# Kernel optimization log

Hardware: AMD Instinct MI355X
Metric: run time of the kernel (lower is better)

Reference implementation:

```python
import jax, jax.numpy as jnp
import numpy as np

C = 256
NUM_HEADS = 8
HEAD_DIM = C // NUM_HEADS
SCALE = HEAD_DIM ** -0.5


def setup_inputs() -> dict:
    key = jax.random.key(0)
    ks = jax.random.split(key, 10)
    B, H, W = 2, 64, 64
    s = 0.02
    return {
        "spatial_feat": jax.random.normal(ks[0], (B, C, H, W), jnp.float32),
        "freq_feat": jax.random.normal(ks[1], (B, C, H, W), jnp.float32),
        "wq": jax.random.normal(ks[2], (C, C), jnp.float32) * s,
        "bq": jax.random.normal(ks[3], (C,), jnp.float32) * s,
        "wk": jax.random.normal(ks[4], (C, C), jnp.float32) * s,
        "bk": jax.random.normal(ks[5], (C,), jnp.float32) * s,
        "wv": jax.random.normal(ks[6], (C, C), jnp.float32) * s,
        "bv": jax.random.normal(ks[7], (C,), jnp.float32) * s,
        "wo": jax.random.normal(ks[8], (C, C), jnp.float32) * s,
        "bo": jax.random.normal(ks[9], (C,), jnp.float32) * s,
    }


def _proj(x, w, b):
    # 1x1 conv == channel-mixing matmul: (O,C) x (B,C,H,W) -> (B,O,H,W)
    return jnp.einsum('oc,bchw->bohw', w, x) + b[None, :, None, None]


def _heads(x, B, HW):
    return x.reshape(B, NUM_HEADS, HEAD_DIM, HW)


def _cross_attend(q_src, kv_src, wq, bq, wk, bk, wv, bv, wo, bo):
    B, Cc, H, W = q_src.shape
    HW = H * W
    q = _heads(_proj(q_src, wq, bq), B, HW)   # (B, h, d, N)
    k = _heads(_proj(kv_src, wk, bk), B, HW)
    v = _heads(_proj(kv_src, wv, bv), B, HW)
    # attn[b,h,m,n] = q[...,m] . k[...,n]
    attn = jnp.einsum('bhdm,bhdn->bhmn', q, k) * SCALE
    attn = jax.nn.softmax(attn, axis=-1)
    # out[...,m] = sum_n v[...,n] * attn[m,n]
    out = jnp.einsum('bhdn,bhmn->bhdm', v, attn)
    out = out.reshape(B, Cc, H, W)
    return _proj(out, wo, bo)


def reference(spatial_feat, freq_feat, wq, bq, wk, bk, wv, bv, wo, bo):
    spatial_attended = spatial_feat + _cross_attend(
        spatial_feat, freq_feat, wq, bq, wk, bk, wv, bv, wo, bo)
    freq_attended = freq_feat + _cross_attend(
        freq_feat, spatial_feat, wq, bq, wk, bk, wv, bv, wo, bo)
    return spatial_attended + freq_attended
```

## Files before the change

kernel.cpp:

```cpp
#include <hip/hip_runtime.h>
#include <hip/hip_bf16.h>

#define B_ 2
#define C_ 256
#define NH_ 8
#define D_ 32
#define N_ 4096
#define SCALE_ 0.17677669529663689f
#define QSC_ 0.25505277f

typedef __hip_bfloat16 bf16;
typedef __attribute__((ext_vector_type(8))) short sx8;
typedef __attribute__((ext_vector_type(4))) short sx4;
typedef __attribute__((ext_vector_type(4))) float fx4;
typedef __attribute__((ext_vector_type(4))) int ix4;

__device__ __forceinline__ float b2f(bf16 x) { return __bfloat162float(x); }
__device__ __forceinline__ bf16 f2b(float x) { return __float2bfloat16(x); }
__device__ __forceinline__ short fbs(float x) { bf16 h = __float2bfloat16(x); return *(short*)&h; }
__device__ __forceinline__ float sbf(short s) { bf16 h = *(bf16*)&s; return __bfloat162float(h); }

#if __has_builtin(__builtin_amdgcn_exp2f)
__device__ __forceinline__ float fexp2(float x) { return __builtin_amdgcn_exp2f(x); }
#else
__device__ __forceinline__ float fexp2(float x) { return exp2f(x); }
#endif

__device__ __forceinline__ unsigned pkbf_tr(float x, float y) {
#if __has_builtin(__builtin_amdgcn_perm)
  return __builtin_amdgcn_perm(__builtin_bit_cast(unsigned, y),
                               __builtin_bit_cast(unsigned, x), 0x07060302u);
#else
  unsigned a = __builtin_bit_cast(unsigned, x) >> 16;
  unsigned b = __builtin_bit_cast(unsigned, y) & 0xFFFF0000u;
  return a | b;
#endif
}
__device__ __forceinline__ void pl32swap(unsigned &a, unsigned &b) {
  asm volatile("v_permlane32_swap_b32 %0, %1" : "+v"(a), "+v"(b));
}
__device__ __forceinline__ void pl16swap(unsigned &a, unsigned &b) {
  asm volatile("v_permlane16_swap_b32 %0, %1" : "+v"(a), "+v"(b));
}

__global__ __launch_bounds__(256)
void convert_kernel(const float* __restrict__ spatial,
                    const float* __restrict__ freq,
                    const float* __restrict__ wq, const float* __restrict__ wk,
                    const float* __restrict__ wv, const float* __restrict__ wo,
                    bf16* __restrict__ xb, bf16* __restrict__ wb,
                    bf16* __restrict__ wob) {
  const int tid = threadIdx.x;
  if (blockIdx.z == 4) {
    int base = (blockIdx.y * 64 + blockIdx.x) * 256 + tid;
    #pragma unroll
    for (int i = 0; i < 4; ++i) {
      int idx = base + i * 65536;
      if (idx < 196608) {
        const float* src = (idx < 65536) ? wq : (idx < 131072) ? wk : wv;
        wb[idx] = f2b(src[idx & 65535]);
      } else {
        wob[idx - 196608] = f2b(wo[idx - 196608]);
      }
    }
    return;
  }

  const int p0 = blockIdx.x * 64;
  const int c0 = blockIdx.y * 64;
  const int z  = blockIdx.z;
  const int s = z >> 1, b = z & 1;
  const float* x = (s == 0) ? spatial : freq;

  __shared__ float ls[64][65];

  const int pp = tid & 63, cb = tid >> 6;
  #pragma unroll
  for (int i = 0; i < 16; ++i) {
    int c = cb + 4 * i;
    ls[c][pp] = x[(size_t)(b * C_ + c0 + c) * N_ + p0 + pp];
  }
  __syncthreads();

  #pragma unroll
  for (int i = 0; i < 2; ++i) {
    int j = tid + 256 * i;
    int p = j >> 3, ck = (j & 7) * 8;
    short tmp[8];
    #pragma unroll
    for (int u = 0; u < 8; ++u) tmp[u] = fbs(ls[ck + u][p]);
    *(sx8*)(xb + ((size_t)z * N_ + p0 + p) * C_ + c0 + ck) = *(sx8*)tmp;
  }
}

__global__ __launch_bounds__(256)
void qkv_gemm_kernel(const bf16* __restrict__ wb, const bf16* __restrict__ xb,
                     const float* __restrict__ bq, const float* __restrict__ bk,
                     const float* __restrict__ bv,
                     bf16* __restrict__ qhf, bf16* __restrict__ khf,
                     bf16* __restrict__ vhf) {
  const int tid = threadIdx.x;
  const int p0 = blockIdx.x * 128;
  const int o0 = blockIdx.y * 128;
  const int z  = blockIdx.z;

  const int lane = tid & 63, w = tid >> 6;
  const int ml = lane & 15, Q4 = (lane >> 4) * 4, Q8 = (lane >> 4) * 8;
  const int ow = (w >> 1) * 64, pw = (w & 1) * 64;

  __shared__ __align__(16) short smem[2 * 128 * 72];
  short* asb = smem;
  short* bsb = smem + 128 * 72;
  __shared__ float bias_s[128];

  if (tid < 128) {
    int o = o0 + tid;
    bias_s[tid] = (o < 256) ? bq[o] : (o < 512) ? bk[o - 256] : bv[o - 512];
  }

  const fx4 z4 = {0.f, 0.f, 0.f, 0.f};
  fx4 acc[4][4];
  #pragma unroll
  for (int ot = 0; ot < 4; ++ot)
    #pragma unroll
    for (int pt = 0; pt < 4; ++pt) acc[ot][pt] = z4;

  const int sr = tid >> 1, scu = (tid & 1) * 32;
  for (int k0 = 0; k0 < 256; k0 += 64) {
    __syncthreads();
    #pragma unroll
    for (int u = 0; u < 4; ++u) {
      *(sx8*)&asb[sr * 72 + scu + u * 8] =
          *(const sx8*)&wb[(o0 + sr) * 256 + k0 + scu + u * 8];
      *(sx8*)&bsb[sr * 72 + scu + u * 8] =
          *(const sx8*)(xb + ((size_t)z * N_ + p0 + sr) * C_ + k0 + scu + u * 8);
    }
    __syncthreads();
    #pragma unroll
    for (int kk = 0; kk < 2; ++kk) {
      sx8 af[4], bfr[4];
      #pragma unroll
      for (int t = 0; t < 4; ++t)
        af[t] = *(sx8*)&asb[(ow + t * 16 + ml) * 72 + kk * 32 + Q8];
      #pragma unroll
      for (int t = 0; t < 4; ++t)
        bfr[t] = *(sx8*)&bsb[(pw + t * 16 + ml) * 72 + kk * 32 + Q8];
      #pragma unroll
      for (int ot = 0; ot < 4; ++ot)
        #pragma unroll
        for (int pt = 0; pt < 4; ++pt)
          acc[ot][pt] = __builtin_amdgcn_mfma_f32_16x16x32_bf16(
              af[ot], bfr[pt], acc[ot][pt], 0, 0, 0);
    }
  }

  if (o0 < 512) {
    bf16* dst = (o0 < 256) ? qhf : khf;
    const int ob = (o0 < 256) ? o0 : o0 - 256;
    const float scl = (o0 < 256) ? QSC_ : 1.f;
    #pragma unroll
    for (int ot = 0; ot < 4; ++ot) {
      const int og = ob + ow + ot * 16 + Q4;
      #pragma unroll
      for (int pt = 0; pt < 4; ++pt) {
        int p = p0 + pw + pt * 16 + ml;
        short tmp[4];
        #pragma unroll
        for (int r = 0; r < 4; ++r)
          tmp[r] = fbs((acc[ot][pt][r] + bias_s[ow + ot * 16 + Q4 + r]) * scl);
        *(sx4*)(dst + (((size_t)z * NH_ + (og >> 5)) * N_ + p) * D_ + (og & 31)) =
            *(sx4*)tmp;
      }
    }
  } else {
    __syncthreads();
    #pragma unroll
    for (int ot = 0; ot < 4; ++ot)
      #pragma unroll
      for (int pt = 0; pt < 4; ++pt) {
        int pl = pw + pt * 16 + ml;
        #pragma unroll
        for (int r = 0; r < 4; ++r) {
          int lo = ow + ot * 16 + Q4 + r;
          smem[lo * 136 + pl] = fbs(acc[ot][pt][r] + bias_s[lo]);
        }
      }
    __syncthreads();
    const int rho0 = o0 - 512;
    #pragma unroll
    for (int i = 0; i < 8; ++i) {
      int j = tid + 256 * i;
      int lo = j >> 4, pg = j & 15;
      int rho = rho0 + lo;
      int h = rho >> 5, d = rho & 31;
      int p = p0 + pg * 8;
      size_t basev = ((size_t)z * NH_ + h) * D_ * N_;
      sx8 v = *(sx8*)&smem[lo * 136 + pg * 8];
      *(sx8*)(vhf + basev + (size_t)(p >> 5) * 1024 + (d >> 4) * 512 +
              (d & 15) * 32 + (p & 31)) = v;
    }
  }
}

__device__ __forceinline__ void attn_tile(const sx8 kf[4], const sx8 vf[2][2],
                                          const sx8 qf[4], sx8 onesf,
                                          fx4 acc[4][2], fx4 lacc[4]) {
  const fx4 z4 = {0.f, 0.f, 0.f, 0.f};
  #pragma unroll
  for (int s4 = 0; s4 < 4; ++s4) {
    fx4 st[4];
    __builtin_amdgcn_s_setprio(1);
    #pragma unroll
    for (int t = 0; t < 4; ++t)
      st[t] = __builtin_amdgcn_mfma_f32_16x16x32_bf16(kf[t], qf[s4], z4, 0, 0, 0);
    __builtin_amdgcn_s_setprio(0);

    unsigned T[4][2];
    #pragma unroll
    for (int t = 0; t < 4; ++t) {
      float e0 = fexp2(st[t][0]), e1 = fexp2(st[t][1]);
      float e2 = fexp2(st[t][2]), e3 = fexp2(st[t][3]);
      T[t][0] = pkbf_tr(e0, e1);
      T[t][1] = pkbf_tr(e2, e3);
    }
    pl32swap(T[0][0], T[1][0]); pl16swap(T[0][0], T[1][0]);
    pl32swap(T[0][1], T[1][1]); pl16swap(T[0][1], T[1][1]);
    pl32swap(T[2][0], T[3][0]); pl16swap(T[2][0], T[3][0]);
    pl32swap(T[2][1], T[3][1]); pl16swap(T[2][1], T[3][1]);
    ix4 p0 = {(int)T[0][0], (int)T[0][1], (int)T[1][0], (int)T[1][1]};
    ix4 p1 = {(int)T[2][0], (int)T[2][1], (int)T[3][0], (int)T[3][1]};
    sx8 pf0 = *(sx8*)&p0;
    sx8 pf1 = *(sx8*)&p1;

    __builtin_amdgcn_s_setprio(1);
    lacc[s4] = __builtin_amdgcn_mfma_f32_16x16x32_bf16(onesf, pf0, lacc[s4], 0, 0, 0);
    lacc[s4] = __builtin_amdgcn_mfma_f32_16x16x32_bf16(onesf, pf1, lacc[s4], 0, 0, 0);
    #pragma unroll
    for (int dt = 0; dt < 2; ++dt) {
      fx4 a = acc[s4][dt];
      a = __builtin_amdgcn_mfma_f32_16x16x32_bf16(vf[dt][0], pf0, a, 0, 0, 0);
      a = __builtin_amdgcn_mfma_f32_16x16x32_bf16(vf[dt][1], pf1, a, 0, 0, 0);
      acc[s4][dt] = a;
    }
    __builtin_amdgcn_s_setprio(0);
  }
}

__global__ __launch_bounds__(256, 2)
void attn_kernel(const bf16* __restrict__ qhf, const bf16* __restrict__ khf,
                 const bf16* __restrict__ vhf, bf16* __restrict__ attoT) {
  const int tid  = threadIdx.x;
  const int m0   = blockIdx.x * 256;
  const int h    = blockIdx.y;
  const int z    = blockIdx.z;
  const int s = z >> 1, b = z & 1;
  const int zo = ((1 - s) << 1) | b;

  const bf16* qz = qhf + ((size_t)z  * NH_ + h) * N_ * D_;
  const bf16* kz = khf + ((size_t)zo * NH_ + h) * N_ * D_;
  const bf16* vz = vhf + ((size_t)zo * NH_ + h) * D_ * N_;

  const int lane = tid & 63;
  const int w    = tid >> 6;
  const int ml   = lane & 15;
  const int q4   = lane >> 4;
  const int Q4   = q4 * 4;
  const int Q8   = q4 * 8;

  sx8 qf[4];
  #pragma unroll
  for (int s4 = 0; s4 < 4; ++s4)
    qf[s4] = *(const sx8*)(qz + (size_t)(m0 + w * 64 + s4 * 16 + ml) * D_ + Q8);

  sx8 onesf;
  #pragma unroll
  for (int u = 0; u < 8; ++u) onesf[u] = (short)0x3F80;

  const fx4 z4 = {0.f, 0.f, 0.f, 0.f};
  fx4 acc[4][2];
  #pragma unroll
  for (int s4 = 0; s4 < 4; ++s4) { acc[s4][0] = z4; acc[s4][1] = z4; }
  fx4 lacc[4] = {z4, z4, z4, z4};

  const bf16* kbase = kz + (size_t)ml * D_ + Q8;
  const bf16* vbase = vz + (size_t)ml * 32 + Q8;

#define LDK(n0, kf)                                                          \
  {                                                                          \
    _Pragma("unroll") for (int t = 0; t < 4; ++t)                            \
        kf[t] = *(const sx8*)(kbase + (size_t)((n0) + t * 16) * D_);         \
  }
#define LDV(n0, vf)                                                          \
  {                                                                          \
    _Pragma("unroll") for (int dt = 0; dt < 2; ++dt)                         \
        _Pragma("unroll") for (int c = 0; c < 2; ++c)                        \
            vf[dt][c] = *(const sx8*)(vbase +                                \
                (size_t)(((n0) >> 5) + c) * 1024 + dt * 512);                \
  }

  sx8 kfA[4], kfB[4], vfA[2][2], vfB[2][2];
  LDK(0, kfA);
  LDV(0, vfA);

  #pragma unroll 1
  for (int n0 = 0; n0 < N_; n0 += 128) {
    const int nn = n0 + 64;
    LDK(nn, kfB);
    LDV(nn, vfB);
    attn_tile(kfA, vfA, qf, onesf, acc, lacc);

    const int nn2 = (nn + 64 < N_) ? nn + 64 : 0;
    LDK(nn2, kfA);
    LDV(nn2, vfA);
    attn_tile(kfB, vfB, qf, onesf, acc, lacc);
  }
#undef LDK
#undef LDV

  #pragma unroll
  for (int s4 = 0; s4 < 4; ++s4) {
    float inv = 1.f / lacc[s4][0];
    int col = m0 + w * 64 + s4 * 16 + ml;
    #pragma unroll
    for (int dt = 0; dt < 2; ++dt) {
      short tmp[4];
      #pragma unroll
      for (int r = 0; r < 4; ++r) tmp[r] = fbs(acc[s4][dt][r] * inv);
      *(sx4*)(attoT + ((size_t)z * N_ + col) * C_ + h * D_ + dt * 16 + Q4) =
          *(sx4*)tmp;
    }
  }
}

__global__ __launch_bounds__(256)
void out_proj_kernel(const bf16* __restrict__ wob, const bf16* __restrict__ attoT,
                     const float* __restrict__ spatial,
                     const float* __restrict__ freq,
                     const float* __restrict__ bo, float* __restrict__ out) {
  const int tid = threadIdx.x;
  const int p0 = blockIdx.x * 64;
  const int o0 = blockIdx.y * 64;
  const int b  = blockIdx.z;

  const int lane = tid & 63, w = tid >> 6;
  const int ml = lane & 15, Q4 = (lane >> 4) * 4, Q8 = (lane >> 4) * 8;
  const int ow = (w >> 1) * 32, pw = (w & 1) * 32;

  __shared__ __align__(16) short asb[64 * 72];
  __shared__ __align__(16) short bsb[64 * 72];
  __shared__ float bo_s[64];

  if (tid < 64) bo_s[tid] = 2.f * bo[o0 + tid];

  const bf16* at0 = attoT + (size_t)(0 + b) * N_ * C_;
  const bf16* at1 = attoT + (size_t)(2 + b) * N_ * C_;

  const fx4 z4 = {0.f, 0.f, 0.f, 0.f};
  fx4 acc[2][2];
  #pragma unroll
  for (int ot = 0; ot < 2; ++ot)
    #pragma unroll
    for (int pt = 0; pt < 2; ++pt) acc[ot][pt] = z4;

  for (int k0 = 0; k0 < 256; k0 += 64) {
    __syncthreads();
    #pragma unroll
    for (int i = 0; i < 2; ++i) {
      int j = tid + 256 * i;
      int r = j >> 3, cu = (j & 7) * 8;
      *(sx8*)&asb[r * 72 + cu] = *(const sx8*)&wob[(o0 + r) * 256 + k0 + cu];
      sx8 va = *(const sx8*)(at0 + (size_t)(p0 + r) * C_ + k0 + cu);
      sx8 vb2 = *(const sx8*)(at1 + (size_t)(p0 + r) * C_ + k0 + cu);
      short tmp[8];
      #pragma unroll
      for (int u = 0; u < 8; ++u) tmp[u] = fbs(sbf(va[u]) + sbf(vb2[u]));
      *(sx8*)&bsb[r * 72 + cu] = *(sx8*)tmp;
    }
    __syncthreads();
    #pragma unroll
    for (int kk = 0; kk < 2; ++kk) {
      sx8 af[2], bfr[2];
      #pragma unroll
      for (int t = 0; t < 2; ++t)
        af[t] = *(sx8*)&asb[(ow + t * 16 + ml) * 72 + kk * 32 + Q8];
      #pragma unroll
      for (int t = 0; t < 2; ++t)
        bfr[t] = *(sx8*)&bsb[(pw + t * 16 + ml) * 72 + kk * 32 + Q8];
      #pragma unroll
      for (int ot = 0; ot < 2; ++ot)
        #pragma unroll
        for (int pt = 0; pt < 2; ++pt)
          acc[ot][pt] = __builtin_amdgcn_mfma_f32_16x16x32_bf16(
              af[ot], bfr[pt], acc[ot][pt], 0, 0, 0);
    }
  }

  #pragma unroll
  for (int ot = 0; ot < 2; ++ot)
    #pragma unroll
    for (int pt = 0; pt < 2; ++pt) {
      int p = p0 + pw + pt * 16 + ml;
      #pragma unroll
      for (int r = 0; r < 4; ++r) {
        int ol = ow + ot * 16 + Q4 + r;
        size_t off = ((size_t)b * C_ + o0 + ol) * N_ + p;
        out[off] = acc[ot][pt][r] + bo_s[ol] + spatial[off] + freq[off];
      }
    }
}

extern "C" void kernel_launch(void* const* d_in, const int* in_sizes, int n_in,
                              void* d_out, int out_size, void* d_ws, size_t ws_size,
                              hipStream_t stream) {
  const float* spatial = (const float*)d_in[0];
  const float* freq    = (const float*)d_in[1];
  const float* wq = (const float*)d_in[2];
  const float* bq = (const float*)d_in[3];
  const float* wk = (const float*)d_in[4];
  const float* bk = (const float*)d_in[5];
  const float* wv = (const float*)d_in[6];
  const float* bv = (const float*)d_in[7];
  const float* wo = (const float*)d_in[8];
  const float* bo = (const float*)d_in[9];
  float* out = (float*)d_out;

  const size_t SZ = (size_t)2 * B_ * N_ * C_;
  bf16* xb    = (bf16*)d_ws;
  bf16* qhf   = xb + SZ;
  bf16* khf   = qhf + SZ;
  bf16* vhf   = khf + SZ;
  bf16* attoT = vhf + SZ;
  bf16* wb    = attoT + SZ;
  bf16* wob   = wb + 768 * 256;

  convert_kernel<<<dim3(N_ / 64, C_ / 64, 5), 256, 0, stream>>>(
      spatial, freq, wq, wk, wv, wo, xb, wb, wob);
  qkv_gemm_kernel<<<dim3(N_ / 128, 768 / 128, 2 * B_), 256, 0, stream>>>(
      wb, xb, bq, bk, bv, qhf, khf, vhf);
  attn_kernel<<<dim3(N_ / 256, NH_, 2 * B_), 256, 0, stream>>>(
      qhf, khf, vhf, attoT);
  out_proj_kernel<<<dim3(N_ / 64, C_ / 64, B_), 256, 0, stream>>>(
      wob, attoT, spatial, freq, bo, out);
}
```

Baseline: 189.2 us.

## Pre-tile QKV GEMM operands into MFMA fragment layout and load directly from global

The convert kernel now writes the bf16 weights and activations in a 16x32 tiled layout that matches the MFMA fragment order. The QKV GEMM then drops its LDS staging and barriers and loads fragments straight from global memory, double-buffering them in registers across the K chunks. It also adds an occupancy hint of 3 blocks per CU. This removes LDS traffic and synchronisation, but every wave now fetches its own operands from global/L2 with less reuse, and the register pressure rises.

Measured after the change: 193.7 us. 2.4% more time.

```diff
diff --git a/kernel.cpp b/kernel.cpp
--- a/kernel.cpp
+++ b/kernel.cpp
@@ -42,6 +42,7 @@
 __device__ __forceinline__ void pl16swap(unsigned &a, unsigned &b) {
   asm volatile("v_permlane16_swap_b32 %0, %1" : "+v"(a), "+v"(b));
 }
+
 
 __global__ __launch_bounds__(256)
 void convert_kernel(const float* __restrict__ spatial,
@@ -58,7 +59,9 @@
       int idx = base + i * 65536;
       if (idx < 196608) {
         const float* src = (idx < 65536) ? wq : (idx < 131072) ? wk : wv;
-        wb[idx] = f2b(src[idx & 65535]);
+        int o = idx >> 8, c = idx & 255;
+        wb[((o >> 4) * 8 + (c >> 5)) * 512 + (o & 15) * 32 + (c & 31)] =
+            f2b(src[idx & 65535]);
       } else {
         wob[idx - 196608] = f2b(wo[idx - 196608]);
       }
@@ -86,14 +89,17 @@
   for (int i = 0; i < 2; ++i) {
     int j = tid + 256 * i;
     int p = j >> 3, ck = (j & 7) * 8;
+    int pg = p0 + p, cg = c0 + ck;
     short tmp[8];
     #pragma unroll
     for (int u = 0; u < 8; ++u) tmp[u] = fbs(ls[ck + u][p]);
-    *(sx8*)(xb + ((size_t)z * N_ + p0 + p) * C_ + c0 + ck) = *(sx8*)tmp;
-  }
-}
-
-__global__ __launch_bounds__(256)
+    *(sx8*)(xb + (size_t)z * N_ * C_ +
+            (size_t)(((pg >> 4) * 8 + (cg >> 5)) * 512) +
+            (pg & 15) * 32 + (cg & 31)) = *(sx8*)tmp;
+  }
+}
+
+__global__ __launch_bounds__(256, 3)
 void qkv_gemm_kernel(const bf16* __restrict__ wb, const bf16* __restrict__ xb,
                      const float* __restrict__ bq, const float* __restrict__ bk,
                      const float* __restrict__ bv,
@@ -108,9 +114,7 @@
   const int ml = lane & 15, Q4 = (lane >> 4) * 4, Q8 = (lane >> 4) * 8;
   const int ow = (w >> 1) * 64, pw = (w & 1) * 64;
 
-  __shared__ __align__(16) short smem[2 * 128 * 72];
-  short* asb = smem;
-  short* bsb = smem + 128 * 72;
+  __shared__ __align__(16) short esm[128 * 136];
   __shared__ float bias_s[128];
 
   if (tid < 128) {
@@ -125,34 +129,41 @@
     #pragma unroll
     for (int pt = 0; pt < 4; ++pt) acc[ot][pt] = z4;
 
-  const int sr = tid >> 1, scu = (tid & 1) * 32;
-  for (int k0 = 0; k0 < 256; k0 += 64) {
-    __syncthreads();
-    #pragma unroll
-    for (int u = 0; u < 4; ++u) {
-      *(sx8*)&asb[sr * 72 + scu + u * 8] =
-          *(const sx8*)&wb[(o0 + sr) * 256 + k0 + scu + u * 8];
-      *(sx8*)&bsb[sr * 72 + scu + u * 8] =
-          *(const sx8*)(xb + ((size_t)z * N_ + p0 + sr) * C_ + k0 + scu + u * 8);
-    }
-    __syncthreads();
-    #pragma unroll
-    for (int kk = 0; kk < 2; ++kk) {
-      sx8 af[4], bfr[4];
-      #pragma unroll
-      for (int t = 0; t < 4; ++t)
-        af[t] = *(sx8*)&asb[(ow + t * 16 + ml) * 72 + kk * 32 + Q8];
-      #pragma unroll
-      for (int t = 0; t < 4; ++t)
-        bfr[t] = *(sx8*)&bsb[(pw + t * 16 + ml) * 72 + kk * 32 + Q8];
-      #pragma unroll
-      for (int ot = 0; ot < 4; ++ot)
-        #pragma unroll
-        for (int pt = 0; pt < 4; ++pt)
-          acc[ot][pt] = __builtin_amdgcn_mfma_f32_16x16x32_bf16(
-              af[ot], bfr[pt], acc[ot][pt], 0, 0, 0);
-    }
-  }
+  const bf16* ap = wb + (size_t)(o0 + ow) * 256 + ml * 32 + Q8;
+  const bf16* bp = xb + (size_t)z * N_ * C_ + (size_t)(p0 + pw) * 256 + ml * 32 + Q8;
+
+#define LDA(ci, dstf)                                                        \
+  {                                                                          \
+    _Pragma("unroll") for (int t = 0; t < 4; ++t)                            \
+        dstf[t] = *(const sx8*)(ap + t * 4096 + (ci) * 512);                 \
+  }
+#define LDB(ci, dstf)                                                        \
+  {                                                                          \
+    _Pragma("unroll") for (int t = 0; t < 4; ++t)                            \
+        dstf[t] = *(const sx8*)(bp + t * 4096 + (ci) * 512);                 \
+  }
+#define MFMA16(af_, bf_)                                                     \
+  {                                                                          \
+    _Pragma("unroll") for (int ot = 0; ot < 4; ++ot)                         \
+        _Pragma("unroll") for (int pt = 0; pt < 4; ++pt)                     \
+            acc[ot][pt] = __builtin_amdgcn_mfma_f32_16x16x32_bf16(           \
+                af_[ot], bf_[pt], acc[ot][pt], 0, 0, 0);                     \
+  }
+
+  sx8 afA[4], afB[4], bfA[4], bfB[4];
+  LDA(0, afA); LDB(0, bfA);
+  #pragma unroll
+  for (int ci = 0; ci < 8; ci += 2) {
+    if (ci + 1 < 8) { LDA(ci + 1, afB); LDB(ci + 1, bfB); }
+    MFMA16(afA, bfA);
+    if (ci + 2 < 8) { LDA(ci + 2, afA); LDB(ci + 2, bfA); }
+    if (ci + 1 < 8) MFMA16(afB, bfB);
+  }
+#undef LDA
+#undef LDB
+#undef MFMA16
+
+  __syncthreads();
 
   if (o0 < 512) {
     bf16* dst = (o0 < 256) ? qhf : khf;
@@ -173,7 +184,6 @@
       }
     }
   } else {
-    __syncthreads();
     #pragma unroll
     for (int ot = 0; ot < 4; ++ot)
       #pragma unroll
@@ -182,7 +192,7 @@
         #pragma unroll
         for (int r = 0; r < 4; ++r) {
           int lo = ow + ot * 16 + Q4 + r;
-          smem[lo * 136 + pl] = fbs(acc[ot][pt][r] + bias_s[lo]);
+          esm[lo * 136 + pl] = fbs(acc[ot][pt][r] + bias_s[lo]);
         }
       }
     __syncthreads();
@@ -195,7 +205,7 @@
       int h = rho >> 5, d = rho & 31;
       int p = p0 + pg * 8;
       size_t basev = ((size_t)z * NH_ + h) * D_ * N_;
-      sx8 v = *(sx8*)&smem[lo * 136 + pg * 8];
+      sx8 v = *(sx8*)&esm[lo * 136 + pg * 8];
       *(sx8*)(vhf + basev + (size_t)(p >> 5) * 1024 + (d >> 4) * 512 +
               (d & 15) * 32 + (p & 31)) = v;
     }
```

## Store out-proj operands in MFMA-fragment tiled layout and load fragments directly

Applied to the files above, without the earlier changes.

The output-projection weights and the attention outputs are written in a 16x32 fragment-tiled layout, so the out-proj kernel can load MFMA operands straight from global memory with 16-byte vector loads. This drops the shared-memory staging and its barriers, and replaces the bf16 add of the two attention outputs with two MFMAs into the same accumulator. Register double buffering overlaps the next chunk's loads with the current MFMAs. In exchange, the kernel issues twice the MFMAs, does no cross-wave reuse through LDS (each wave reloads its own fragments), and the attention kernel's stores are now scattered.

New measurement: 190.7 us. No clear change (+0.8%).

```diff
diff --git a/kernel.cpp b/kernel.cpp
--- a/kernel.cpp
+++ b/kernel.cpp
@@ -42,6 +42,7 @@
 __device__ __forceinline__ void pl16swap(unsigned &a, unsigned &b) {
   asm volatile("v_permlane16_swap_b32 %0, %1" : "+v"(a), "+v"(b));
 }
+
 
 __global__ __launch_bounds__(256)
 void convert_kernel(const float* __restrict__ spatial,
@@ -60,7 +61,10 @@
         const float* src = (idx < 65536) ? wq : (idx < 131072) ? wk : wv;
         wb[idx] = f2b(src[idx & 65535]);
       } else {
-        wob[idx - 196608] = f2b(wo[idx - 196608]);
+        int r = idx - 196608;
+        int o = r >> 8, c = r & 255;
+        wob[((o >> 4) * 8 + (c >> 5)) * 512 + (o & 15) * 32 + (c & 31)] =
+            f2b(wo[r]);
       }
     }
     return;
@@ -317,6 +321,7 @@
 #undef LDK
 #undef LDV
 
+  bf16* az = attoT + (size_t)z * N_ * C_;
   #pragma unroll
   for (int s4 = 0; s4 < 4; ++s4) {
     float inv = 1.f / lacc[s4][0];
@@ -326,8 +331,8 @@
       short tmp[4];
       #pragma unroll
       for (int r = 0; r < 4; ++r) tmp[r] = fbs(acc[s4][dt][r] * inv);
-      *(sx4*)(attoT + ((size_t)z * N_ + col) * C_ + h * D_ + dt * 16 + Q4) =
-          *(sx4*)tmp;
+      *(sx4*)(az + (size_t)(((col >> 4) * 8 + h) * 512) +
+              (col & 15) * 32 + dt * 16 + Q4) = *(sx4*)tmp;
     }
   }
 }
@@ -346,14 +351,11 @@
   const int ml = lane & 15, Q4 = (lane >> 4) * 4, Q8 = (lane >> 4) * 8;
   const int ow = (w >> 1) * 32, pw = (w & 1) * 32;
 
-  __shared__ __align__(16) short asb[64 * 72];
-  __shared__ __align__(16) short bsb[64 * 72];
   __shared__ float bo_s[64];
-
   if (tid < 64) bo_s[tid] = 2.f * bo[o0 + tid];
 
-  const bf16* at0 = attoT + (size_t)(0 + b) * N_ * C_;
-  const bf16* at1 = attoT + (size_t)(2 + b) * N_ * C_;
+  const bf16* a0 = attoT + (size_t)(0 + b) * N_ * C_;
+  const bf16* a1 = attoT + (size_t)(2 + b) * N_ * C_;
 
   const fx4 z4 = {0.f, 0.f, 0.f, 0.f};
   fx4 acc[2][2];
@@ -362,38 +364,39 @@
     #pragma unroll
     for (int pt = 0; pt < 2; ++pt) acc[ot][pt] = z4;
 
-  for (int k0 = 0; k0 < 256; k0 += 64) {
-    __syncthreads();
-    #pragma unroll
-    for (int i = 0; i < 2; ++i) {
-      int j = tid + 256 * i;
-      int r = j >> 3, cu = (j & 7) * 8;
-      *(sx8*)&asb[r * 72 + cu] = *(const sx8*)&wob[(o0 + r) * 256 + k0 + cu];
-      sx8 va = *(const sx8*)(at0 + (size_t)(p0 + r) * C_ + k0 + cu);
-      sx8 vb2 = *(const sx8*)(at1 + (size_t)(p0 + r) * C_ + k0 + cu);
-      short tmp[8];
-      #pragma unroll
-      for (int u = 0; u < 8; ++u) tmp[u] = fbs(sbf(va[u]) + sbf(vb2[u]));
-      *(sx8*)&bsb[r * 72 + cu] = *(sx8*)tmp;
-    }
-    __syncthreads();
-    #pragma unroll
-    for (int kk = 0; kk < 2; ++kk) {
-      sx8 af[2], bfr[2];
-      #pragma unroll
-      for (int t = 0; t < 2; ++t)
-        af[t] = *(sx8*)&asb[(ow + t * 16 + ml) * 72 + kk * 32 + Q8];
-      #pragma unroll
-      for (int t = 0; t < 2; ++t)
-        bfr[t] = *(sx8*)&bsb[(pw + t * 16 + ml) * 72 + kk * 32 + Q8];
-      #pragma unroll
-      for (int ot = 0; ot < 2; ++ot)
-        #pragma unroll
-        for (int pt = 0; pt < 2; ++pt)
-          acc[ot][pt] = __builtin_amdgcn_mfma_f32_16x16x32_bf16(
-              af[ot], bfr[pt], acc[ot][pt], 0, 0, 0);
-    }
-  }
+  const bf16* ap  = wob + (size_t)((o0 + ow) >> 4) * 4096 + ml * 32 + Q8;
+  const bf16* bp0 = a0  + (size_t)((p0 + pw) >> 4) * 4096 + ml * 32 + Q8;
+  const bf16* bp1 = a1  + (size_t)((p0 + pw) >> 4) * 4096 + ml * 32 + Q8;
+
+#define LDF(base, ci, dstf)                                                  \
+  {                                                                          \
+    _Pragma("unroll") for (int t = 0; t < 2; ++t)                            \
+        dstf[t] = *(const sx8*)((base) + t * 4096 + (ci) * 512);             \
+  }
+#define MFMA8(af_, b0_, b1_)                                                 \
+  {                                                                          \
+    _Pragma("unroll") for (int ot = 0; ot < 2; ++ot)                         \
+        _Pragma("unroll") for (int pt = 0; pt < 2; ++pt) {                   \
+          acc[ot][pt] = __builtin_amdgcn_mfma_f32_16x16x32_bf16(             \
+              af_[ot], b0_[pt], acc[ot][pt], 0, 0, 0);                       \
+          acc[ot][pt] = __builtin_amdgcn_mfma_f32_16x16x32_bf16(             \
+              af_[ot], b1_[pt], acc[ot][pt], 0, 0, 0);                       \
+        }                                                                    \
+  }
+
+  sx8 afA[2], afB[2], b0A[2], b0B[2], b1A[2], b1B[2];
+  LDF(ap, 0, afA); LDF(bp0, 0, b0A); LDF(bp1, 0, b1A);
+  #pragma unroll
+  for (int ci = 0; ci < 8; ci += 2) {
+    if (ci + 1 < 8) { LDF(ap, ci + 1, afB); LDF(bp0, ci + 1, b0B); LDF(bp1, ci + 1, b1B); }
+    MFMA8(afA, b0A, b1A);
+    if (ci + 2 < 8) { LDF(ap, ci + 2, afA); LDF(bp0, ci + 2, b0A); LDF(bp1, ci + 2, b1A); }
+    if (ci + 1 < 8) MFMA8(afB, b0B, b1B);
+  }
+#undef LDF
+#undef MFMA8
+
+  __syncthreads();
 
   #pragma unroll
   for (int ot = 0; ot < 2; ++ot)
```

## Load QKV GEMM tiles via direct global-to-LDS loads with XOR-swizzled layout

Applied to the files above, without the earlier changes.

The QKV projection GEMM now fills its shared-memory tiles with global_load_lds (direct global-to-LDS DMA) instead of loading through registers and storing. Padding is removed, so bank conflicts are instead avoided by XOR-swizzling 8-element chunks. The swizzle is applied upstream when the convert kernel writes the bf16 weights and activations. This cuts VGPR traffic and LDS store instructions, at the cost of coupling the global layout to the swizzle, which any other reader of wb/xb must also honour.

New measurement: 194.4 us. 2.7% more time.

```diff
diff --git a/kernel.cpp b/kernel.cpp
--- a/kernel.cpp
+++ b/kernel.cpp
@@ -14,6 +14,9 @@
 typedef __attribute__((ext_vector_type(4))) short sx4;
 typedef __attribute__((ext_vector_type(4))) float fx4;
 typedef __attribute__((ext_vector_type(4))) int ix4;
+
+typedef __attribute__((address_space(1))) const void gvoid;
+typedef __attribute__((address_space(3))) void lvoid;
 
 __device__ __forceinline__ float b2f(bf16 x) { return __bfloat162float(x); }
 __device__ __forceinline__ bf16 f2b(float x) { return __float2bfloat16(x); }
@@ -42,6 +45,7 @@
 __device__ __forceinline__ void pl16swap(unsigned &a, unsigned &b) {
   asm volatile("v_permlane16_swap_b32 %0, %1" : "+v"(a), "+v"(b));
 }
+
 
 __global__ __launch_bounds__(256)
 void convert_kernel(const float* __restrict__ spatial,
@@ -58,7 +62,8 @@
       int idx = base + i * 65536;
       if (idx < 196608) {
         const float* src = (idx < 65536) ? wq : (idx < 131072) ? wk : wv;
-        wb[idx] = f2b(src[idx & 65535]);
+        int o = idx >> 8, c = idx & 255;
+        wb[(o << 8) | (c ^ ((o & 7) << 3))] = f2b(src[idx & 65535]);
       } else {
         wob[idx - 196608] = f2b(wo[idx - 196608]);
       }
@@ -89,7 +94,8 @@
     short tmp[8];
     #pragma unroll
     for (int u = 0; u < 8; ++u) tmp[u] = fbs(ls[ck + u][p]);
-    *(sx8*)(xb + ((size_t)z * N_ + p0 + p) * C_ + c0 + ck) = *(sx8*)tmp;
+    *(sx8*)(xb + ((size_t)z * N_ + p0 + p) * C_ + c0 +
+            (((j & 7) ^ (p & 7)) * 8)) = *(sx8*)tmp;
   }
 }
 
@@ -106,11 +112,12 @@
 
   const int lane = tid & 63, w = tid >> 6;
   const int ml = lane & 15, Q4 = (lane >> 4) * 4, Q8 = (lane >> 4) * 8;
+  const int q4 = lane >> 4;
   const int ow = (w >> 1) * 64, pw = (w & 1) * 64;
 
-  __shared__ __align__(16) short smem[2 * 128 * 72];
+  __shared__ __align__(16) short smem[128 * 136];
   short* asb = smem;
-  short* bsb = smem + 128 * 72;
+  short* bsb = smem + 128 * 64;
   __shared__ float bias_s[128];
 
   if (tid < 128) {
@@ -125,26 +132,36 @@
     #pragma unroll
     for (int pt = 0; pt < 4; ++pt) acc[ot][pt] = z4;
 
-  const int sr = tid >> 1, scu = (tid & 1) * 32;
+  const int srow = lane >> 3, scol = (lane & 7) * 8;
+  const bf16* agp = wb + (size_t)(o0 + w * 32 + srow) * 256 + scol;
+  const bf16* bgp = xb + ((size_t)z * N_ + p0 + w * 32 + srow) * C_ + scol;
+  const int lbase = (w * 32) * 64;
+
   for (int k0 = 0; k0 < 256; k0 += 64) {
     __syncthreads();
     #pragma unroll
-    for (int u = 0; u < 4; ++u) {
-      *(sx8*)&asb[sr * 72 + scu + u * 8] =
-          *(const sx8*)&wb[(o0 + sr) * 256 + k0 + scu + u * 8];
-      *(sx8*)&bsb[sr * 72 + scu + u * 8] =
-          *(const sx8*)(xb + ((size_t)z * N_ + p0 + sr) * C_ + k0 + scu + u * 8);
+    for (int i = 0; i < 4; ++i) {
+      __builtin_amdgcn_global_load_lds(
+          (gvoid*)(agp + (size_t)(i * 8) * 256 + k0),
+          (lvoid*)&asb[lbase + i * 8 * 64], 16, 0, 0);
+      __builtin_amdgcn_global_load_lds(
+          (gvoid*)(bgp + (size_t)(i * 8) * 256 + k0),
+          (lvoid*)&bsb[lbase + i * 8 * 64], 16, 0, 0);
     }
     __syncthreads();
     #pragma unroll
     for (int kk = 0; kk < 2; ++kk) {
       sx8 af[4], bfr[4];
       #pragma unroll
-      for (int t = 0; t < 4; ++t)
-        af[t] = *(sx8*)&asb[(ow + t * 16 + ml) * 72 + kk * 32 + Q8];
-      #pragma unroll
-      for (int t = 0; t < 4; ++t)
-        bfr[t] = *(sx8*)&bsb[(pw + t * 16 + ml) * 72 + kk * 32 + Q8];
+      for (int t = 0; t < 4; ++t) {
+        int R = ow + t * 16 + ml;
+        af[t] = *(sx8*)&asb[R * 64 + (((kk * 4 + q4) ^ (R & 7)) * 8)];
+      }
+      #pragma unroll
+      for (int t = 0; t < 4; ++t) {
+        int S = pw + t * 16 + ml;
+        bfr[t] = *(sx8*)&bsb[S * 64 + (((kk * 4 + q4) ^ (S & 7)) * 8)];
+      }
       #pragma unroll
       for (int ot = 0; ot < 4; ++ot)
         #pragma unroll
```
